# Performance work log

Hardware: AMD Instinct MI355X
Metric: run time of the kernel (lower is better)

Reference implementation:

```python
import jax, jax.numpy as jnp
import numpy as np

E = 200000      # n_edges
IN = 128        # input_nf
HID = 32        # hidden_nf
H = 4           # att_heads
OUT = 128       # output_nf
MAXK = 16       # MAX_K neighbor slots


def setup_inputs() -> dict:
    key = jax.random.key(0)
    ks = jax.random.split(key, 12)
    Z = jax.random.normal(ks[0], (E, IN), dtype=jnp.float32)
    idx = jax.random.randint(ks[1], (E, 2, MAXK), 0, E)
    red = jax.random.uniform(ks[2], (E, 1, MAXK)) < 0.15
    klist = jnp.where(red, -1, idx).astype(jnp.int64)
    s = 0.05  # xavier-ish scale
    Wq = jax.random.normal(ks[3], (H, HID, IN), dtype=jnp.float32) * s
    Wk = jax.random.normal(ks[4], (H, HID, IN), dtype=jnp.float32) * s
    Wv = jax.random.normal(ks[5], (H, HID, IN), dtype=jnp.float32) * s
    Wb = jax.random.normal(ks[6], (H, 1, IN), dtype=jnp.float32) * s
    Wg = jax.random.normal(ks[7], (H, HID, IN), dtype=jnp.float32) * s
    bg = jnp.zeros((H, HID), dtype=jnp.float32)
    Wout = jax.random.normal(ks[8], (OUT, H * HID), dtype=jnp.float32) * s
    bout = jnp.zeros((OUT,), dtype=jnp.float32)
    return {"Z": Z, "klist": klist, "Wq": Wq, "Wk": Wk, "Wv": Wv,
            "Wb": Wb, "Wg": Wg, "bg": bg, "Wout": Wout, "bout": bout}


def reference(Z, klist, Wq, Wk, Wv, Wb, Wg, bg, Wout, bout):
    idx_i, idx_j = klist[:, 0], klist[:, 1]          # (E, K)
    red = idx_i == -1
    valid = (~red).astype(Z.dtype)[..., None]        # (E, K, 1)
    ii = jnp.where(red, 0, idx_i)
    jj = jnp.where(red, 0, idx_j)
    scale = 1.0 / np.sqrt(HID)
    outs = []
    for h in range(H):  # att_heads: small fixed loop over structurally distinct heads
        q = Z @ Wq[h].T                              # (E, HID)
        k = Z @ Wk[h].T
        v = Z @ Wv[h].T
        b = (Z @ Wb[h].T)[:, 0]                      # (E,)
        g = jax.nn.sigmoid(Z @ Wg[h].T + bg[h])      # (E, HID)
        tri_k = jnp.take(k, ii, axis=0) * valid      # (E, K, HID), redundant slots zeroed
        tri_v = jnp.take(v, ii, axis=0) * valid
        tri_b = jnp.take(b, jj, axis=0) * valid[..., 0]  # (E, K)
        scores = scale * jnp.einsum('eh,ekh->ek', q, tri_k) + tri_b
        alpha = jax.nn.softmax(scores, axis=1)       # (E, K)
        att = jnp.einsum('ek,ekh->eh', alpha, tri_v) # (E, HID)
        outs.append(g * att)
    out = jnp.concatenate(outs, axis=-1) @ Wout.T + bout  # (E, OUT)
    # dropout is identity in eval mode
    return out
```

## Files before the change

### kernel.cpp

```cpp
#include <hip/hip_runtime.h>
#include <hip/hip_bf16.h>
#include <stdint.h>

#define EDGES 200000
#define INF   128
#define HID   32
#define NHEAD 4
#define OUTF  128
#define MAXK  16

#define NPAD  528

#define XPAD  136

typedef unsigned short u16;
typedef __attribute__((ext_vector_type(8))) short bf16x8;
typedef __attribute__((ext_vector_type(4))) float f32x4;

__device__ __forceinline__ u16 f2bf(float f) {
  union { float f; uint32_t u; } v; v.f = f;
  uint32_t u = v.u;
  return (u16)((u + 0x7FFFu + ((u >> 16) & 1u)) >> 16);
}
__device__ __forceinline__ float bflo(uint32_t p) {
  union { uint32_t u; float f; } v; v.u = p << 16;
  return v.f;
}
__device__ __forceinline__ float bfhi(uint32_t p) {
  union { uint32_t u; float f; } v; v.u = p & 0xFFFF0000u;
  return v.f;
}

__device__ __forceinline__ uint32_t cvtpk_bf16(float lo, float hi) {
  float2 t; t.x = lo; t.y = hi;
  __hip_bfloat162 h = __float22bfloat162_rn(t);
  uint32_t u;
  __builtin_memcpy(&u, &h, 4);
  return u;
}
__device__ __forceinline__ bf16x8 pack8(float4 f0, float4 f1) {
  union { uint32_t u[4]; bf16x8 v; } r;
  r.u[0] = cvtpk_bf16(f0.x, f0.y);
  r.u[1] = cvtpk_bf16(f0.z, f0.w);
  r.u[2] = cvtpk_bf16(f1.x, f1.y);
  r.u[3] = cvtpk_bf16(f1.z, f1.w);
  return r.v;
}
__device__ __forceinline__ float sigm(float x) {
  return 1.0f / (1.0f + __expf(-x));
}

template <int CTRL>
__device__ __forceinline__ float dpp_add(float x) {
  int y = __builtin_amdgcn_update_dpp(0, __builtin_bit_cast(int, x),
                                      CTRL, 0xF, 0xF, true);
  return x + __builtin_bit_cast(float, y);
}
__device__ __forceinline__ float row16_sum(float x) {
  x = dpp_add<0xB1>(x);
  x = dpp_add<0x4E>(x);
  x = dpp_add<0x141>(x);
  x = dpp_add<0x140>(x);
  return x;
}

struct AccPair { f32x4 a, b; };
__device__ __forceinline__ AccPair tile_mm(const u16* __restrict__ W, int row0,
                                           int ml, int blk,
                                           const bf16x8 (&zfr)[2][4], int ldw) {
  bf16x8 wfr[4];
#pragma unroll
  for (int kk = 0; kk < 4; ++kk)
    wfr[kk] = *(const bf16x8*)(W + (size_t)(row0 + ml) * ldw + kk * 32 + blk * 8);
  AccPair r;
  r.a = (f32x4){0.f, 0.f, 0.f, 0.f};
  r.b = (f32x4){0.f, 0.f, 0.f, 0.f};
#pragma unroll
  for (int kk = 0; kk < 4; ++kk) {
    r.a = __builtin_amdgcn_mfma_f32_16x16x32_bf16(wfr[kk], zfr[0][kk], r.a, 0, 0, 0);
    r.b = __builtin_amdgcn_mfma_f32_16x16x32_bf16(wfr[kk], zfr[1][kk], r.b, 0, 0, 0);
  }
  return r;
}

__device__ __forceinline__ void load_zfr(const float* __restrict__ Z, long e0,
                                         int ml, int blk, bf16x8 (&zfr)[2][4]) {
#pragma unroll
  for (int s = 0; s < 2; ++s) {
    const float* zp = Z + (e0 + s * 16 + ml) * INF + blk * 8;
#pragma unroll
    for (int kk = 0; kk < 4; ++kk) {
      float4 f0 = *(const float4*)(zp + kk * 32);
      float4 f1 = *(const float4*)(zp + kk * 32 + 4);
      zfr[s][kk] = pack8(f0, f1);
    }
  }
}

__device__ __forceinline__ void ds_stage_pair(u16* sb, int ml, int blk, int t,
                                              uint2 pa, uint2 pb) {
  const int col2 = (t * 16 + blk * 4) * 2;
  const int swz = (ml & 7) << 4;
  *(uint2*)((char*)sb + ((ml * 128 + col2) ^ swz)) = pa;
  *(uint2*)((char*)sb + (((16 + ml) * 128 + col2) ^ swz)) = pb;
}
__device__ __forceinline__ void flush_group(const u16* sb, int lane,
                                            u16* __restrict__ dst, long e0,
                                            int rowu16, int colu16) {
  const int rr = lane >> 3;
  const int c8 = (lane & 7) * 8;
#pragma unroll
  for (int i = 0; i < 4; ++i) {
    const int row = i * 8 + rr;
    bf16x8 v = *(const bf16x8*)((const char*)sb +
                                ((row * 128 + c8 * 2) ^ ((row & 7) << 4)));
    *(bf16x8*)(dst + (e0 + row) * rowu16 + colu16 + c8) = v;
  }
}

__global__ __launch_bounds__(256) void prep_kernel(
    const float* __restrict__ Wq, const float* __restrict__ Wk,
    const float* __restrict__ Wv, const float* __restrict__ Wb,
    const float* __restrict__ Wg, const float* __restrict__ Wout,
    u16* __restrict__ Wc, u16* __restrict__ Woutb)
{
  int t = blockIdx.x * 256 + threadIdx.x;
  if (t < NPAD * INF) {
    int n = t >> 7, k = t & 127;
    float v = 0.0f;
    if (n < 128)       v = Wq[n * 128 + k];
    else if (n < 256)  v = Wg[(n - 128) * 128 + k];
    else if (n < 512) {
      int m = n - 256, h = m >> 6, c = m & 63;
      v = (c < 32) ? Wk[(h * 32 + c) * 128 + k] : Wv[(h * 32 + (c - 32)) * 128 + k];
    } else if (n < 516) v = Wb[(n - 512) * 128 + k];
    Wc[t] = f2bf(v);
  } else if (t < NPAD * INF + OUTF * 128) {
    int u = t - NPAD * INF;
    Woutb[u] = f2bf(Wout[u]);
  }
}

__global__ __launch_bounds__(256) void proj_kernel(
    const float* __restrict__ Z, const u16* __restrict__ Wc,
    u16* __restrict__ kvb, float* __restrict__ bb)
{
  __shared__ u16 stage[4][2048];

  const int wid = threadIdx.x >> 6, lane = threadIdx.x & 63;
  const int ml = lane & 15, blk = lane >> 4;
  const int pairId = wid >> 1;
  const int half   = wid & 1;
  const long e0 = (long)blockIdx.x * 64 + pairId * 32;

  bf16x8 zfr[2][4];
  load_zfr(Z, e0, ml, blk, zfr);

  for (int g = 0; g < 2; ++g) {
    const int gg = half * 2 + g;
    u16* sb = stage[wid];
#pragma unroll
    for (int t = 0; t < 4; ++t) {
      AccPair acc = tile_mm(Wc, 256 + (gg * 4 + t) * 16, ml, blk, zfr, INF);
      uint2 pa, pb;
      pa.x = cvtpk_bf16(acc.a[0], acc.a[1]); pa.y = cvtpk_bf16(acc.a[2], acc.a[3]);
      pb.x = cvtpk_bf16(acc.b[0], acc.b[1]); pb.y = cvtpk_bf16(acc.b[2], acc.b[3]);
      ds_stage_pair(sb, ml, blk, t, pa, pb);
    }
    flush_group(sb, lane, kvb, e0, 256, gg * 64);
  }

  if (half == 1) {
    AccPair acc = tile_mm(Wc, 512, ml, blk, zfr, INF);
    if (blk == 0) {
      *(float4*)(bb + (e0 + ml) * 4) =
          make_float4(acc.a[0], acc.a[1], acc.a[2], acc.a[3]);
      *(float4*)(bb + (e0 + 16 + ml) * 4) =
          make_float4(acc.b[0], acc.b[1], acc.b[2], acc.b[3]);
    }
  }
}

__global__ __launch_bounds__(256) void attn_out_kernel(
    const float* __restrict__ Z, const u16* __restrict__ Wc,
    const float* __restrict__ bg,
    const int* __restrict__ klist, const u16* __restrict__ kvb,
    const float* __restrict__ bb, const u16* __restrict__ Woutb,
    const float* __restrict__ bout, float* __restrict__ out)
{
  __shared__ u16 qs[32 * XPAD];
  __shared__ u16 gs[32 * XPAD];

  const int wid = threadIdx.x >> 6;
  const int lane = threadIdx.x & 63;
  const long e0 = (long)blockIdx.x * 32;
  const int ml = lane & 15, blk = lane >> 4;

  {
    bf16x8 zfr[2][4];
    load_zfr(Z, e0, ml, blk, zfr);

#pragma unroll
    for (int t = 0; t < 2; ++t) {
      const int nt = wid * 2 + t;
      AccPair acc = tile_mm(Wc, nt * 16, ml, blk, zfr, INF);
      const int n0 = nt * 16 + blk * 4;
      uint2 pa, pb;
      pa.x = cvtpk_bf16(acc.a[0], acc.a[1]); pa.y = cvtpk_bf16(acc.a[2], acc.a[3]);
      pb.x = cvtpk_bf16(acc.b[0], acc.b[1]); pb.y = cvtpk_bf16(acc.b[2], acc.b[3]);
      *(uint2*)(&qs[ml * XPAD + n0]) = pa;
      *(uint2*)(&qs[(16 + ml) * XPAD + n0]) = pb;
    }
#pragma unroll
    for (int t = 0; t < 2; ++t) {
      const int nt = wid * 2 + t;
      AccPair acc = tile_mm(Wc, 128 + nt * 16, ml, blk, zfr, INF);
      const int n0 = nt * 16 + blk * 4;
      float4 b4 = *(const float4*)(bg + n0);
      uint2 pa, pb;
      pa.x = cvtpk_bf16(sigm(acc.a[0] + b4.x), sigm(acc.a[1] + b4.y));
      pa.y = cvtpk_bf16(sigm(acc.a[2] + b4.z), sigm(acc.a[3] + b4.w));
      pb.x = cvtpk_bf16(sigm(acc.b[0] + b4.x), sigm(acc.b[1] + b4.y));
      pb.y = cvtpk_bf16(sigm(acc.b[2] + b4.z), sigm(acc.b[3] + b4.w));
      *(uint2*)(&gs[ml * XPAD + n0]) = pa;
      *(uint2*)(&gs[(16 + ml) * XPAD + n0]) = pb;
    }
  }
  __syncthreads();

  const int h = lane >> 4;
  const int kvo = h * 64 + (lane & 15) * 2;
  const float scale = 0.17677669529663687f;

#pragma unroll 1
  for (int it = 0; it < 8; ++it) {
    const int le = wid * 8 + it;
    int e = (int)e0 + le;
    e = __builtin_amdgcn_readfirstlane(e);

    const uint32_t q2 = *(const uint32_t*)(&qs[le * XPAD + 2 * lane]);
    const uint32_t g2 = *(const uint32_t*)(&gs[le * XPAD + 2 * lane]);
    const float q0 = bflo(q2), q1 = bfhi(q2);

    float sc[MAXK];
    uint32_t vvm[MAXK];
    const int* kl = klist + (size_t)e * 32;
#pragma unroll
    for (int nb = 0; nb < MAXK; ++nb) {
      const int ii = kl[nb];
      const int jj = kl[16 + nb];
      const bool valid = (ii >= 0);
      const int is = valid ? ii : 0;
      const int js = valid ? jj : 0;
      const u16* kvrow = kvb + (size_t)is * 256;
      uint32_t kki = *(const uint32_t*)(kvrow + kvo);
      uint32_t vvi = *(const uint32_t*)(kvrow + kvo + 32);
      float p = q0 * bflo(kki) + q1 * bfhi(kki);
      p = row16_sum(p);
      float bj = bb[(size_t)js * 4 + h];
      sc[nb]  = valid ? (scale * p + bj) : 0.0f;
      vvm[nb] = valid ? vvi : 0u;
    }

    float m = sc[0];
#pragma unroll
    for (int nb = 1; nb < MAXK; ++nb) m = fmaxf(m, sc[nb]);
    float s = 0.f, a0 = 0.f, a1 = 0.f;
#pragma unroll
    for (int nb = 0; nb < MAXK; ++nb) {
      float al = __expf(sc[nb] - m);
      s += al;
      a0 += al * bflo(vvm[nb]);
      a1 += al * bfhi(vvm[nb]);
    }
    float inv = 1.0f / s;
    uint32_t xo = cvtpk_bf16(bflo(g2) * a0 * inv, bfhi(g2) * a1 * inv);
    *(uint32_t*)(&qs[le * XPAD + 2 * lane]) = xo;
  }

  __syncthreads();

  bf16x8 xfr[2][4];
#pragma unroll
  for (int s = 0; s < 2; ++s) {
#pragma unroll
    for (int kk = 0; kk < 4; ++kk)
      xfr[s][kk] = *(const bf16x8*)(&qs[(s * 16 + ml) * XPAD + kk * 32 + blk * 8]);
  }

  const long eA = e0 + ml, eB = e0 + 16 + ml;

#pragma unroll
  for (int t = 0; t < 2; ++t) {
    const int nt = wid * 2 + t;
    AccPair acc = tile_mm(Woutb, nt * 16, ml, blk, xfr, 128);
    const int o0 = nt * 16 + blk * 4;
    float4 b4 = *(const float4*)(bout + o0);
    float4 ra = make_float4(acc.a[0] + b4.x, acc.a[1] + b4.y,
                            acc.a[2] + b4.z, acc.a[3] + b4.w);
    float4 rb = make_float4(acc.b[0] + b4.x, acc.b[1] + b4.y,
                            acc.b[2] + b4.z, acc.b[3] + b4.w);
    *(float4*)(out + eA * 128 + o0) = ra;
    *(float4*)(out + eB * 128 + o0) = rb;
  }
}

extern "C" void kernel_launch(void* const* d_in, const int* in_sizes, int n_in,
                              void* d_out, int out_size, void* d_ws, size_t ws_size,
                              hipStream_t stream) {
  const float* Z     = (const float*)d_in[0];
  const int*   klist = (const int*)  d_in[1];
  const float* Wq    = (const float*)d_in[2];
  const float* Wk    = (const float*)d_in[3];
  const float* Wv    = (const float*)d_in[4];
  const float* Wb    = (const float*)d_in[5];
  const float* Wg    = (const float*)d_in[6];
  const float* bg    = (const float*)d_in[7];
  const float* Wout  = (const float*)d_in[8];
  const float* bout  = (const float*)d_in[9];
  float* out = (float*)d_out;

  char* ws = (char*)d_ws;
  u16*   Wc    = (u16*)(ws);
  u16*   Woutb = (u16*)(ws + 135168);
  u16*   kvb   = (u16*)(ws + 167936);
  float* bb    = (float*)(ws + 102567936);

  prep_kernel<<<(NPAD * INF + OUTF * 128 + 255) / 256, 256, 0, stream>>>(
      Wq, Wk, Wv, Wb, Wg, Wout, Wc, Woutb);
  proj_kernel<<<EDGES / 64, 256, 0, stream>>>(
      Z, Wc, kvb, bb);
  attn_out_kernel<<<EDGES / 32, 256, 0, stream>>>(
      Z, Wc, bg, klist, kvb, bb, Woutb, bout, out);
}
```

Measured before the change: 504.1 us.

## Interleave K/V columns, fold log2e into scores, nontemporal Z/out, smaller proj blocks

Reorders the packed K/V weight columns so each lane's key pair and value pair sit next to each other, letting the gather do one 8-byte load per neighbour instead of two 4-byte loads. Folds log2(e) into the scale and the stored bias so softmax can use exp2 in place of exp. Loads Z and stores the output with nontemporal hints to reduce cache pollution. Changes the projection kernel to 32 edges per block, one wave per K/V group, doubling the grid and giving the bias tile to a single wave. The attention gather is likely the dominant cost, so fewer memory transactions there is the main intended gain.

```diff
diff --git a/kernel.cpp b/kernel.cpp
--- a/kernel.cpp
+++ b/kernel.cpp
@@ -13,6 +13,9 @@
 
 #define XPAD  136
 
+#define LOG2E 1.44269504088896f
+#define SCALE2 0.2550348612f
+
 typedef unsigned short u16;
 typedef __attribute__((ext_vector_type(8))) short bf16x8;
 typedef __attribute__((ext_vector_type(4))) float f32x4;
@@ -38,12 +41,12 @@
   __builtin_memcpy(&u, &h, 4);
   return u;
 }
-__device__ __forceinline__ bf16x8 pack8(float4 f0, float4 f1) {
+__device__ __forceinline__ bf16x8 pack8(f32x4 f0, f32x4 f1) {
   union { uint32_t u[4]; bf16x8 v; } r;
-  r.u[0] = cvtpk_bf16(f0.x, f0.y);
-  r.u[1] = cvtpk_bf16(f0.z, f0.w);
-  r.u[2] = cvtpk_bf16(f1.x, f1.y);
-  r.u[3] = cvtpk_bf16(f1.z, f1.w);
+  r.u[0] = cvtpk_bf16(f0[0], f0[1]);
+  r.u[1] = cvtpk_bf16(f0[2], f0[3]);
+  r.u[2] = cvtpk_bf16(f1[0], f1[1]);
+  r.u[3] = cvtpk_bf16(f1[2], f1[3]);
   return r.v;
 }
 __device__ __forceinline__ float sigm(float x) {
@@ -90,8 +93,8 @@
     const float* zp = Z + (e0 + s * 16 + ml) * INF + blk * 8;
 #pragma unroll
     for (int kk = 0; kk < 4; ++kk) {
-      float4 f0 = *(const float4*)(zp + kk * 32);
-      float4 f1 = *(const float4*)(zp + kk * 32 + 4);
+      f32x4 f0 = __builtin_nontemporal_load((const f32x4*)(zp + kk * 32));
+      f32x4 f1 = __builtin_nontemporal_load((const f32x4*)(zp + kk * 32 + 4));
       zfr[s][kk] = pack8(f0, f1);
     }
   }
@@ -131,8 +134,9 @@
     if (n < 128)       v = Wq[n * 128 + k];
     else if (n < 256)  v = Wg[(n - 128) * 128 + k];
     else if (n < 512) {
-      int m = n - 256, h = m >> 6, c = m & 63;
-      v = (c < 32) ? Wk[(h * 32 + c) * 128 + k] : Wv[(h * 32 + (c - 32)) * 128 + k];
+      int c = n - 256, h = c >> 6, r = c & 63, ml = r >> 2, j = r & 3;
+      int d = 2 * ml + (j & 1);
+      v = (j < 2) ? Wk[(h * 32 + d) * 128 + k] : Wv[(h * 32 + d) * 128 + k];
     } else if (n < 516) v = Wb[(n - 512) * 128 + k];
     Wc[t] = f2bf(v);
   } else if (t < NPAD * INF + OUTF * 128) {
@@ -149,34 +153,33 @@
 
   const int wid = threadIdx.x >> 6, lane = threadIdx.x & 63;
   const int ml = lane & 15, blk = lane >> 4;
-  const int pairId = wid >> 1;
-  const int half   = wid & 1;
-  const long e0 = (long)blockIdx.x * 64 + pairId * 32;
+  const long e0 = (long)blockIdx.x * 32;
 
   bf16x8 zfr[2][4];
   load_zfr(Z, e0, ml, blk, zfr);
 
-  for (int g = 0; g < 2; ++g) {
-    const int gg = half * 2 + g;
+  {
     u16* sb = stage[wid];
 #pragma unroll
     for (int t = 0; t < 4; ++t) {
-      AccPair acc = tile_mm(Wc, 256 + (gg * 4 + t) * 16, ml, blk, zfr, INF);
+      AccPair acc = tile_mm(Wc, 256 + (wid * 4 + t) * 16, ml, blk, zfr, INF);
       uint2 pa, pb;
       pa.x = cvtpk_bf16(acc.a[0], acc.a[1]); pa.y = cvtpk_bf16(acc.a[2], acc.a[3]);
       pb.x = cvtpk_bf16(acc.b[0], acc.b[1]); pb.y = cvtpk_bf16(acc.b[2], acc.b[3]);
       ds_stage_pair(sb, ml, blk, t, pa, pb);
     }
-    flush_group(sb, lane, kvb, e0, 256, gg * 64);
-  }
-
-  if (half == 1) {
+    flush_group(sb, lane, kvb, e0, 256, wid * 64);
+  }
+
+  if (wid == 3) {
     AccPair acc = tile_mm(Wc, 512, ml, blk, zfr, INF);
     if (blk == 0) {
-      *(float4*)(bb + (e0 + ml) * 4) =
-          make_float4(acc.a[0], acc.a[1], acc.a[2], acc.a[3]);
-      *(float4*)(bb + (e0 + 16 + ml) * 4) =
-          make_float4(acc.b[0], acc.b[1], acc.b[2], acc.b[3]);
+      *(f32x4*)(bb + (e0 + ml) * 4) =
+          (f32x4){acc.a[0] * LOG2E, acc.a[1] * LOG2E,
+                  acc.a[2] * LOG2E, acc.a[3] * LOG2E};
+      *(f32x4*)(bb + (e0 + 16 + ml) * 4) =
+          (f32x4){acc.b[0] * LOG2E, acc.b[1] * LOG2E,
+                  acc.b[2] * LOG2E, acc.b[3] * LOG2E};
     }
   }
 }
@@ -216,12 +219,12 @@
       const int nt = wid * 2 + t;
       AccPair acc = tile_mm(Wc, 128 + nt * 16, ml, blk, zfr, INF);
       const int n0 = nt * 16 + blk * 4;
-      float4 b4 = *(const float4*)(bg + n0);
+      f32x4 b4 = *(const f32x4*)(bg + n0);
       uint2 pa, pb;
-      pa.x = cvtpk_bf16(sigm(acc.a[0] + b4.x), sigm(acc.a[1] + b4.y));
-      pa.y = cvtpk_bf16(sigm(acc.a[2] + b4.z), sigm(acc.a[3] + b4.w));
-      pb.x = cvtpk_bf16(sigm(acc.b[0] + b4.x), sigm(acc.b[1] + b4.y));
-      pb.y = cvtpk_bf16(sigm(acc.b[2] + b4.z), sigm(acc.b[3] + b4.w));
+      pa.x = cvtpk_bf16(sigm(acc.a[0] + b4[0]), sigm(acc.a[1] + b4[1]));
+      pa.y = cvtpk_bf16(sigm(acc.a[2] + b4[2]), sigm(acc.a[3] + b4[3]));
+      pb.x = cvtpk_bf16(sigm(acc.b[0] + b4[0]), sigm(acc.b[1] + b4[1]));
+      pb.y = cvtpk_bf16(sigm(acc.b[2] + b4[2]), sigm(acc.b[3] + b4[3]));
       *(uint2*)(&gs[ml * XPAD + n0]) = pa;
       *(uint2*)(&gs[(16 + ml) * XPAD + n0]) = pb;
     }
@@ -229,8 +232,7 @@
   __syncthreads();
 
   const int h = lane >> 4;
-  const int kvo = h * 64 + (lane & 15) * 2;
-  const float scale = 0.17677669529663687f;
+  const int kvo = h * 64 + (lane & 15) * 4;
 
 #pragma unroll 1
   for (int it = 0; it < 8; ++it) {
@@ -252,14 +254,12 @@
       const bool valid = (ii >= 0);
       const int is = valid ? ii : 0;
       const int js = valid ? jj : 0;
-      const u16* kvrow = kvb + (size_t)is * 256;
-      uint32_t kki = *(const uint32_t*)(kvrow + kvo);
-      uint32_t vvi = *(const uint32_t*)(kvrow + kvo + 32);
-      float p = q0 * bflo(kki) + q1 * bfhi(kki);
+      uint2 kv4 = *(const uint2*)(kvb + (size_t)is * 256 + kvo);
+      float p = q0 * bflo(kv4.x) + q1 * bfhi(kv4.x);
       p = row16_sum(p);
       float bj = bb[(size_t)js * 4 + h];
-      sc[nb]  = valid ? (scale * p + bj) : 0.0f;
-      vvm[nb] = valid ? vvi : 0u;
+      sc[nb]  = valid ? fmaf(SCALE2, p, bj) : 0.0f;
+      vvm[nb] = valid ? kv4.y : 0u;
     }
 
     float m = sc[0];
@@ -268,7 +268,7 @@
     float s = 0.f, a0 = 0.f, a1 = 0.f;
 #pragma unroll
     for (int nb = 0; nb < MAXK; ++nb) {
-      float al = __expf(sc[nb] - m);
+      float al = exp2f(sc[nb] - m);
       s += al;
       a0 += al * bflo(vvm[nb]);
       a1 += al * bfhi(vvm[nb]);
@@ -295,13 +295,13 @@
     const int nt = wid * 2 + t;
     AccPair acc = tile_mm(Woutb, nt * 16, ml, blk, xfr, 128);
     const int o0 = nt * 16 + blk * 4;
-    float4 b4 = *(const float4*)(bout + o0);
-    float4 ra = make_float4(acc.a[0] + b4.x, acc.a[1] + b4.y,
-                            acc.a[2] + b4.z, acc.a[3] + b4.w);
-    float4 rb = make_float4(acc.b[0] + b4.x, acc.b[1] + b4.y,
-                            acc.b[2] + b4.z, acc.b[3] + b4.w);
-    *(float4*)(out + eA * 128 + o0) = ra;
-    *(float4*)(out + eB * 128 + o0) = rb;
+    f32x4 b4 = *(const f32x4*)(bout + o0);
+    f32x4 ra = (f32x4){acc.a[0] + b4[0], acc.a[1] + b4[1],
+                       acc.a[2] + b4[2], acc.a[3] + b4[3]};
+    f32x4 rb = (f32x4){acc.b[0] + b4[0], acc.b[1] + b4[1],
+                       acc.b[2] + b4[2], acc.b[3] + b4[3]};
+    __builtin_nontemporal_store(ra, (f32x4*)(out + eA * 128 + o0));
+    __builtin_nontemporal_store(rb, (f32x4*)(out + eB * 128 + o0));
   }
 }
 
@@ -328,7 +328,7 @@
 
   prep_kernel<<<(NPAD * INF + OUTF * 128 + 255) / 256, 256, 0, stream>>>(
       Wq, Wk, Wv, Wb, Wg, Wout, Wc, Woutb);
-  proj_kernel<<<EDGES / 64, 256, 0, stream>>>(
+  proj_kernel<<<EDGES / 32, 256, 0, stream>>>(
       Z, Wc, kvb, bb);
   attn_out_kernel<<<EDGES / 32, 256, 0, stream>>>(
       Z, Wc, bg, klist, kvb, bb, Woutb, bout, out);
```

Result: slower. 992.7 us (+96.9%).
